# Kernel optimization log

Hardware: AMD Instinct MI355X
Metric: run time of the kernel (lower is better)

The kernel has to match this reference:

```python
import jax, jax.numpy as jnp
import numpy as np

N_NODES = 50000
N_EDGES = 800000
D_IN = 8
D_MODEL = 128
N_CLASSES = 2


def gcn_conv(x, W, b, src, dst, n_nodes):
    # PyG GCNConv: h = x @ W; add self-loops; D^{-1/2} A D^{-1/2} aggregation; + bias
    h = x @ W  # [N, D]
    deg = jax.ops.segment_sum(jnp.ones(src.shape[0], h.dtype), dst, num_segments=n_nodes) + 1.0  # +1 self-loop
    dinv = jax.lax.rsqrt(deg)  # deg >= 1 always
    norm = dinv[src] * dinv[dst]  # [E]
    agg = jax.ops.segment_sum(h[src] * norm[:, None], dst, num_segments=n_nodes)
    agg = agg + h * (dinv * dinv)[:, None]  # self-loop term, norm_ii = dinv_i^2
    return agg + b


def setup_inputs() -> dict:
    key = jax.random.key(0)
    ks = jax.random.split(key, 10)
    x = jax.random.normal(ks[0], (N_NODES, D_IN), jnp.float32)
    edge_index = jax.random.randint(ks[1], (2, N_EDGES), 0, N_NODES, jnp.int64 if jax.config.jax_enable_x64 else jnp.int32)
    def glorot(k, shape):
        lim = np.sqrt(6.0 / (shape[0] + shape[1]))
        return jax.random.uniform(k, shape, jnp.float32, -lim, lim)
    return {
        "x": x,
        "edge_index": edge_index,
        "W1": glorot(ks[2], (D_IN, D_MODEL)),
        "b1": jnp.zeros((D_MODEL,), jnp.float32),
        "W2": glorot(ks[3], (D_MODEL, D_MODEL)),
        "b2": jnp.zeros((D_MODEL,), jnp.float32),
        "Wlin1": glorot(ks[4], (2 * D_MODEL, D_MODEL)),
        "blin1": jnp.zeros((D_MODEL,), jnp.float32),
        "Wfin": glorot(ks[5], (D_MODEL, N_CLASSES)),
        "bfin": jnp.zeros((N_CLASSES,), jnp.float32),
    }


def reference(x, edge_index, W1, b1, W2, b2, Wlin1, blin1, Wfin, bfin):
    src, dst = edge_index[0], edge_index[1]
    n = x.shape[0]
    h = jax.nn.relu(gcn_conv(x, W1, b1, src, dst, n))
    h = jax.nn.relu(gcn_conv(h, W2, b2, src, dst, n))
    xpair = jnp.concatenate((h[src], h[dst]), axis=1)  # [E, 2*D]
    xpair = jax.nn.relu(xpair @ Wlin1 + blin1)
    logits = xpair @ Wfin + bfin  # [E, C]
    return jax.nn.log_softmax(logits, axis=1)
```

## Files before the change

kernel.cpp:

```cpp
#include <hip/hip_runtime.h>
#include <stdint.h>
#include <math.h>

#define D 128

typedef unsigned short u16;
typedef __attribute__((ext_vector_type(8))) short bf16x8;
typedef __attribute__((ext_vector_type(4))) float f32x4;
typedef __attribute__((ext_vector_type(2))) float f32x2;

union BU { uint4 u; bf16x8 s; };

__device__ __forceinline__ unsigned f2bf_pk(float a, float b) {
    union { float f; unsigned u; } x, y; x.f = a; y.f = b;
    unsigned ra = x.u + 0x7FFF + ((x.u >> 16) & 1);
    unsigned rb = y.u + 0x7FFF + ((y.u >> 16) & 1);
    return (ra >> 16) | (rb & 0xFFFF0000u);
}
__device__ __forceinline__ u16 f2bf(float f) {
    union { float f; unsigned u; } x; x.f = f;
    unsigned r = x.u + 0x7FFF + ((x.u >> 16) & 1);
    return (u16)(r >> 16);
}
__device__ __forceinline__ f32x2 bf2f2v(unsigned u) {
    union { unsigned w[2]; f32x2 v; } t;
    t.w[0] = u << 16; t.w[1] = u & 0xFFFF0000u;
    return t.v;
}
__device__ __forceinline__ f32x2 vmax0(f32x2 a) {
    return __builtin_elementwise_max(a, (f32x2)(0.f));
}
__device__ __forceinline__ int padded4(int deg) {
    return (deg + 3) & ~3;
}


__global__ __launch_bounds__(256) void k_degree8(const int* __restrict__ dst, int E,
                                                 int* __restrict__ hist8, int N) {
    int i = blockIdx.x * 256 + threadIdx.x;
    int copy = blockIdx.x & 7;
    int E4 = E >> 2;
    if (i < E4) {
        int4 d = ((const int4*)dst)[i];
        int* h = hist8 + copy * N;
        atomicAdd(&h[d.x], 1);
        atomicAdd(&h[d.y], 1);
        atomicAdd(&h[d.z], 1);
        atomicAdd(&h[d.w], 1);
    }
    if (i == 0) {
        for (int j = E4 * 4; j < E; ++j) atomicAdd(&hist8[dst[j]], 1);
    }
}

__global__ __launch_bounds__(256) void k_xcdoff_bsum(int* __restrict__ hist8, int* __restrict__ degi,
                                                     float* __restrict__ dinv, int* __restrict__ bsum, int N) {
    __shared__ int ws[4];
    int t = threadIdx.x;
    int i = blockIdx.x * 256 + t;
    int pd = 0;
    if (i < N) {
        int run = 0;
#pragma unroll
        for (int j = 0; j < 8; ++j) {
            int c = hist8[j * N + i];
            hist8[j * N + i] = run;
            run += c;
        }
        degi[i] = run;
        dinv[i] = rsqrtf((float)run + 1.0f);
        pd = padded4(run);
    }
    int v = pd;
#pragma unroll
    for (int off = 1; off < 64; off <<= 1) v += __shfl_xor(v, off, 64);
    if ((t & 63) == 0) ws[t >> 6] = v;
    __syncthreads();
    if (t == 0) bsum[blockIdx.x] = ws[0] + ws[1] + ws[2] + ws[3];
}

__global__ __launch_bounds__(1024) void k_boff_wprep(const int* __restrict__ bsum, int* __restrict__ boff,
                                                     int nb, int* __restrict__ prow, int N,
                                                     const float* __restrict__ W2, const float* __restrict__ Wlin,
                                                     unsigned* __restrict__ wswz) {
    int t = threadIdx.x;
    if (blockIdx.x == 0) {
        __shared__ int s[1024];
        s[t] = (t < nb) ? bsum[t] : 0;
        __syncthreads();
        for (int off = 1; off < 1024; off <<= 1) {
            int v = (t >= off) ? s[t - off] : 0;
            __syncthreads();
            s[t] += v;
            __syncthreads();
        }
        if (t < nb) boff[t] = (t == 0) ? 0 : s[t - 1];
        if (t == 0) prow[N] = s[1023];
    } else {
        int tid = (blockIdx.x - 1) * 1024 + t;
        int m = tid >> 13;
        int r = tid & 8191;
        int jp = r & 3;
        int lane = (r >> 2) & 63;
        int ct = (r >> 8) & 7;
        int kc = r >> 11;
        int k0 = kc * 32 + (lane >> 4) * 8 + 2 * jp;
        int n = ct * 16 + (lane & 15);
        const float* srcp = (m == 0) ? W2 : (Wlin + (m - 1) * 16384);
        wswz[tid] = f2bf_pk(srcp[k0 * 128 + n], srcp[(k0 + 1) * 128 + n]);
    }
}

__global__ __launch_bounds__(256) void k_scan_final(const int* __restrict__ degi, const int* __restrict__ boff,
                                                    int* __restrict__ prow, int N) {
    __shared__ int s[256];
    int t = threadIdx.x;
    int i = blockIdx.x * 256 + t;
    int pd = (i < N) ? padded4(degi[i]) : 0;
    s[t] = pd;
    __syncthreads();
    for (int off = 1; off < 256; off <<= 1) {
        int v = (t >= off) ? s[t - off] : 0;
        __syncthreads();
        s[t] += v;
        __syncthreads();
    }
    if (i < N) prow[i] = boff[blockIdx.x] + ((t == 0) ? 0 : s[t - 1]);
}


__global__ __launch_bounds__(256) void k_scatter_fill_xform(
        const int* __restrict__ src, const int* __restrict__ dst, int E,
        const int* __restrict__ prow, int* __restrict__ hist8, const int* __restrict__ degi,
        int2* __restrict__ coleid, int N, int eb4, int nb,
        const float* __restrict__ x, const float* __restrict__ W1,
        const float* __restrict__ dinv, unsigned* __restrict__ g) {
    __shared__ float Ws[8 * D];
    int t = threadIdx.x;
    int b = blockIdx.x;
    if (b < eb4) {
        int i = b * 256 + t;
        int copy = b & 7;
        int E4 = E >> 2;
        if (i < E4) {
            int4 d = ((const int4*)dst)[i];
            int4 s4 = ((const int4*)src)[i];
            int* h = hist8 + copy * N;
            int e = i * 4;
            int off;
            off = atomicAdd(&h[d.x], 1); coleid[prow[d.x] + off] = make_int2(s4.x, e + 0);
            off = atomicAdd(&h[d.y], 1); coleid[prow[d.y] + off] = make_int2(s4.y, e + 1);
            off = atomicAdd(&h[d.z], 1); coleid[prow[d.z] + off] = make_int2(s4.z, e + 2);
            off = atomicAdd(&h[d.w], 1); coleid[prow[d.w] + off] = make_int2(s4.w, e + 3);
        }
        if (i == 0) {
            for (int j = E4 * 4; j < E; ++j) {
                int d = dst[j];
                int off = atomicAdd(&hist8[d], 1);
                coleid[prow[d] + off] = make_int2(src[j], j);
            }
        }
    } else if (b < eb4 + nb) {
        int n = (b - eb4) * 256 + t;
        if (n < N) {
            int lo = prow[n];
            int deg = degi[n];
            int pd = padded4(deg);
            for (int j = deg; j < pd; ++j) coleid[lo + j] = make_int2(N, 0);
        }
        if (b == eb4 && t == 0) {
            int P = prow[N];
            for (int j = 0; j < 16; ++j) coleid[P + j] = make_int2(N, 0);
        }
    } else {
        int xb0 = b - eb4 - nb;
        for (int i = t; i < 8 * D; i += 256) Ws[i] = W1[i];
        __syncthreads();
        int node = xb0 * 4 + (t >> 6);
        int l = t & 63;
        if (node < N) {
            float s0 = 0.f, s1 = 0.f;
#pragma unroll
            for (int k = 0; k < 8; ++k) {
                float xv = x[node * 8 + k];
                s0 += xv * Ws[k * D + 2 * l];
                s1 += xv * Ws[k * D + 2 * l + 1];
            }
            float di = dinv[node];
            g[node * 64 + l] = f2bf_pk(s0 * di, s1 * di);
        }
        if (xb0 == 0 && t < 64) g[(size_t)N * 64 + t] = 0;
    }
}


#define HROW 136

template <bool DUAL>
__global__ __launch_bounds__(256) void k_aggemm(const uint4* __restrict__ g, const int* __restrict__ prow,
                                                const int2* __restrict__ coleid, const float* __restrict__ dinv,
                                                const float* __restrict__ biasH,
                                                const uint4* __restrict__ wB0, const uint4* __restrict__ wB1,
                                                const float* __restrict__ bias1,
                                                u16* __restrict__ out0, u16* __restrict__ out1, int N) {
    __shared__ u16 hs[16 * HROW];
    int t = threadIdx.x;
    int wv = t >> 6;
    int lane = t & 63;
    int sub = lane >> 4;
    int r = lane & 15;
    int base = blockIdx.x * 16;

    for (int nd = 0; nd < 4; ++nd) {
        int i = base + wv * 4 + nd;
        int lrow = wv * 4 + nd;
        if (i < N) {
            f32x2 acc2[4];
#pragma unroll
            for (int j = 0; j < 4; ++j) acc2[j] = (f32x2)(0.f);
            int lo = prow[i], hiP = prow[i + 1];
            int idx = lo + sub;
            int c0 = coleid[idx].x;
            int c1 = (idx + 4 < hiP) ? coleid[idx + 4].x : N;
            int c2 = (idx + 8 < hiP) ? coleid[idx + 8].x : N;
            uint4 v0 = g[c0 * 16 + r];
            uint4 v1 = g[c1 * 16 + r];
            for (int k = lo; k < hiP; k += 4) {
                int c3 = (idx + 12 < hiP) ? coleid[idx + 12].x : N;
                uint4 v2 = g[c2 * 16 + r];
                acc2[0] += bf2f2v(v0.x);
                acc2[1] += bf2f2v(v0.y);
                acc2[2] += bf2f2v(v0.z);
                acc2[3] += bf2f2v(v0.w);
                v0 = v1; v1 = v2; c2 = c3; idx += 4;
            }
#pragma unroll
            for (int j = 0; j < 4; ++j) {
                acc2[j].x += __shfl_xor(acc2[j].x, 16, 64);
                acc2[j].y += __shfl_xor(acc2[j].y, 16, 64);
                acc2[j].x += __shfl_xor(acc2[j].x, 32, 64);
                acc2[j].y += __shfl_xor(acc2[j].y, 32, 64);
            }
            if (sub == 0) {
                uint4 sv = g[i * 16 + r];
                acc2[0] += bf2f2v(sv.x);
                acc2[1] += bf2f2v(sv.y);
                acc2[2] += bf2f2v(sv.z);
                acc2[3] += bf2f2v(sv.w);
                float di = dinv[i];
                float4 b0 = ((const float4*)biasH)[r * 2];
                float4 b1v = ((const float4*)biasH)[r * 2 + 1];
                float r0 = fmaxf(acc2[0].x * di + b0.x, 0.f);
                float r1 = fmaxf(acc2[0].y * di + b0.y, 0.f);
                float r2 = fmaxf(acc2[1].x * di + b0.z, 0.f);
                float r3 = fmaxf(acc2[1].y * di + b0.w, 0.f);
                float r4 = fmaxf(acc2[2].x * di + b1v.x, 0.f);
                float r5 = fmaxf(acc2[2].y * di + b1v.y, 0.f);
                float r6 = fmaxf(acc2[3].x * di + b1v.z, 0.f);
                float r7 = fmaxf(acc2[3].y * di + b1v.w, 0.f);
                uint4 o;
                o.x = f2bf_pk(r0, r1);
                o.y = f2bf_pk(r2, r3);
                o.z = f2bf_pk(r4, r5);
                o.w = f2bf_pk(r6, r7);
                *(uint4*)(hs + lrow * HROW + r * 8) = o;
            }
        } else if (sub == 0) {
            *(uint4*)(hs + lrow * HROW + r * 8) = make_uint4(0, 0, 0, 0);
        }
    }
    __syncthreads();

    int quad = lane >> 4;
    int l15 = lane & 15;
    int ct0 = wv * 2;

    f32x4 accA[2], accB[2];
#pragma unroll
    for (int q = 0; q < 2; ++q) { accA[q] = (f32x4){0.f, 0.f, 0.f, 0.f}; accB[q] = (f32x4){0.f, 0.f, 0.f, 0.f}; }

    const uint4* hrow = (const uint4*)(hs + l15 * HROW);
#pragma unroll
    for (int kc = 0; kc < 4; ++kc) {
        BU a; a.u = hrow[kc * 4 + quad];
#pragma unroll
        for (int q = 0; q < 2; ++q) {
            BU b0; b0.u = wB0[(kc * 8 + ct0 + q) * 64 + lane];
            accA[q] = __builtin_amdgcn_mfma_f32_16x16x32_bf16(a.s, b0.s, accA[q], 0, 0, 0);
            if (DUAL) {
                BU b1; b1.u = wB1[(kc * 8 + ct0 + q) * 64 + lane];
                accB[q] = __builtin_amdgcn_mfma_f32_16x16x32_bf16(a.s, b1.s, accB[q], 0, 0, 0);
            }
        }
    }
#pragma unroll
    for (int reg = 0; reg < 4; ++reg) {
        int node = base + quad * 4 + reg;
        if (node >= N) continue;
        float sc = DUAL ? 1.0f : dinv[node];
#pragma unroll
        for (int q = 0; q < 2; ++q) {
            int colj = (ct0 + q) * 16 + l15;
            out0[(size_t)node * 128 + colj] = f2bf(accA[q][reg] * sc);
            if (DUAL) out1[(size_t)node * 128 + colj] = f2bf(accB[q][reg] + bias1[colj]);
        }
    }
    if (blockIdx.x == 0 && t < 64) ((unsigned*)out0)[(size_t)N * 64 + t] = 0;
}


__global__ __launch_bounds__(256) void k_edge(const uint4* __restrict__ a, const uint4* __restrict__ c,
                                              const int* __restrict__ prow, const int* __restrict__ degi,
                                              const int2* __restrict__ coleid,
                                              const float* __restrict__ Wfin, const float* __restrict__ bfin,
                                              float* __restrict__ out, int N) {
    int wave = (blockIdx.x * blockDim.x + threadIdx.x) >> 6;
    int lane = threadIdx.x & 63;
    if (wave >= N) return;
    int d = wave;
    int g = lane >> 4;
    int r = lane & 15;

    f32x2 wf0v[4], wf1v[4];
    const float4* wvp = (const float4*)Wfin;
#pragma unroll
    for (int q = 0; q < 4; ++q) {
        float4 m = wvp[r * 4 + q];
        wf0v[q] = (f32x2){m.x, m.z};
        wf1v[q] = (f32x2){m.y, m.w};
    }
    float bf0 = bfin[0], bf1 = bfin[1];

    f32x2 cf2[4];
    {
        uint4 cv = c[d * 16 + r];
        cf2[0] = bf2f2v(cv.x);
        cf2[1] = bf2f2v(cv.y);
        cf2[2] = bf2f2v(cv.z);
        cf2[3] = bf2f2v(cv.w);
    }

    int lo = prow[d], hiP = prow[d + 1];
    int deg = degi[d];

    int idx = lo + g;
    int2 q0 = coleid[idx];
    int2 q1 = coleid[idx + 4];
    int c1 = (idx + 4 < hiP) ? q1.x : N;
    int2 q2 = coleid[idx + 8];
    int c2 = (idx + 8 < hiP) ? q2.x : N;
    int e0 = q0.y, e1 = q1.y, e2 = q2.y;
    uint4 v0 = a[q0.x * 16 + r];
    uint4 v1 = a[c1 * 16 + r];

    int rel = g;
    for (int k = lo; k < hiP; k += 4) {
        int2 q3 = coleid[idx + 12];
        int c3 = (idx + 12 < hiP) ? q3.x : N;
        uint4 v2 = a[c2 * 16 + r];
        f32x2 p0v = (f32x2)(0.f), p1v = (f32x2)(0.f);
        f32x2 z;
        z = vmax0(bf2f2v(v0.x) + cf2[0]); p0v += z * wf0v[0]; p1v += z * wf1v[0];
        z = vmax0(bf2f2v(v0.y) + cf2[1]); p0v += z * wf0v[1]; p1v += z * wf1v[1];
        z = vmax0(bf2f2v(v0.z) + cf2[2]); p0v += z * wf0v[2]; p1v += z * wf1v[2];
        z = vmax0(bf2f2v(v0.w) + cf2[3]); p0v += z * wf0v[3]; p1v += z * wf1v[3];
        float p0 = p0v.x + p0v.y;
        float p1 = p1v.x + p1v.y;
        p0 += __shfl_xor(p0, 1, 64);
        p0 += __shfl_xor(p0, 2, 64);
        p0 += __shfl_xor(p0, 4, 64);
        p0 += __shfl_xor(p0, 8, 64);
        p1 += __shfl_xor(p1, 1, 64);
        p1 += __shfl_xor(p1, 2, 64);
        p1 += __shfl_xor(p1, 4, 64);
        p1 += __shfl_xor(p1, 8, 64);
        if (r == 0 && rel < deg) {
            float l0 = p0 + bf0, l1 = p1 + bf1;
            float m = fmaxf(l0, l1);
            float lse = m + __logf(__expf(l0 - m) + __expf(l1 - m));
            *((float2*)(out + 2 * (size_t)e0)) = make_float2(l0 - lse, l1 - lse);
        }
        v0 = v1; v1 = v2;
        e0 = e1; e1 = e2; e2 = q3.y;
        c2 = c3; idx += 4; rel += 4;
    }
}

extern "C" void kernel_launch(void* const* d_in, const int* in_sizes, int n_in,
                              void* d_out, int out_size, void* d_ws, size_t ws_size,
                              hipStream_t stream) {
    const float* x     = (const float*)d_in[0];
    const int*   ei    = (const int*)d_in[1];
    const float* W1    = (const float*)d_in[2];
    const float* b1    = (const float*)d_in[3];
    const float* W2    = (const float*)d_in[4];
    const float* b2    = (const float*)d_in[5];
    const float* Wlin1 = (const float*)d_in[6];
    const float* blin1 = (const float*)d_in[7];
    const float* Wfin  = (const float*)d_in[8];
    const float* bfin  = (const float*)d_in[9];
    float* out = (float*)d_out;

    int N = in_sizes[0] / 8;
    int E = in_sizes[1] / 2;
    const int* src = ei;
    const int* dst = ei + E;
    int nb = (N + 255) / 256;
    int eb4 = (E / 4 + 255) / 256;
    int xb = (N + 3) / 4;

    char* w = (char*)d_ws;
    int* hist8 = (int*)w;     w += (size_t)8 * N * 4;
    int* degi = (int*)w;      w += (size_t)N * 4;
    int* prow = (int*)w;      w += (size_t)(N + 1) * 4;
    float* dinv = (float*)w;  w += (size_t)N * 4;
    int* bsum = (int*)w;      w += (size_t)nb * 4;
    int* boff = (int*)w;      w += (size_t)nb * 4;
    w = (char*)(((uintptr_t)w + 255) & ~(uintptr_t)255);
    int2* coleid = (int2*)w;  w += ((size_t)E + 8 * (size_t)N + 64) * 8;
    unsigned* wswz = (unsigned*)w; w += (size_t)3 * 8192 * 4;
    unsigned* bufG = (unsigned*)w; w += (size_t)(N + 1) * 64 * 4;
    unsigned* bufA = (unsigned*)w; w += (size_t)(N + 1) * 64 * 4;
    unsigned* bufC = (unsigned*)w; w += (size_t)N * 64 * 4;
    unsigned* bufG2 = (unsigned*)w; w += (size_t)(N + 1) * 64 * 4;

    hipMemsetAsync(hist8, 0, (size_t)8 * N * 4, stream);

    k_degree8<<<eb4, 256, 0, stream>>>(dst, E, hist8, N);
    k_xcdoff_bsum<<<nb, 256, 0, stream>>>(hist8, degi, dinv, bsum, N);
    k_boff_wprep<<<25, 1024, 0, stream>>>(bsum, boff, nb, prow, N, W2, Wlin1, wswz);
    k_scan_final<<<nb, 256, 0, stream>>>(degi, boff, prow, N);
    k_scatter_fill_xform<<<eb4 + nb + xb, 256, 0, stream>>>(src, dst, E, prow, hist8, degi,
                                                            coleid, N, eb4, nb, x, W1, dinv, bufG);

    int ablocks = (N + 15) / 16;
    k_aggemm<false><<<ablocks, 256, 0, stream>>>((const uint4*)bufG, prow, coleid, dinv, b1,
                                                 (const uint4*)wswz, nullptr, nullptr,
                                                 (u16*)bufG2, nullptr, N);
    k_aggemm<true><<<ablocks, 256, 0, stream>>>((const uint4*)bufG2, prow, coleid, dinv, b2,
                                                (const uint4*)(wswz + 8192), (const uint4*)(wswz + 16384),
                                                blin1, (u16*)bufA, (u16*)bufC, N);

    k_edge<<<(N + 3) / 4, 256, 0, stream>>>((const uint4*)bufA, (const uint4*)bufC,
                                            prow, degi, coleid, Wfin, bfin, out, N);
}
```

Baseline: 294.3 us.

## Replace 8 private degree histograms with destination-range-partitioned single histogram

Instead of eight replicated histogram copies (one per block group) that must be prefix-combined, each edge chunk is now read by eight blocks, each owning one eighth of the destination-node range and doing atomics only into that slice of a single histogram. This removes the 8xN histogram memset, the per-node combine pass and the degi array, and keeps each part's atomics within a narrow address range, presumably to improve L2 locality per XCD. In exchange the dst array is read eight times, and src is read once for each part that has a hit, both in the degree pass and the scatter pass.

```diff
diff --git a/kernel.cpp b/kernel.cpp
--- a/kernel.cpp
+++ b/kernel.cpp
@@ -35,39 +35,32 @@
 }
 
 
-__global__ __launch_bounds__(256) void k_degree8(const int* __restrict__ dst, int E,
-                                                 int* __restrict__ hist8, int N) {
-    int i = blockIdx.x * 256 + threadIdx.x;
-    int copy = blockIdx.x & 7;
-    int E4 = E >> 2;
-    if (i < E4) {
+__global__ __launch_bounds__(256) void k_degree_part(const int* __restrict__ dst, int E,
+                                                     int* __restrict__ hist, int N8, int G4) {
+    int b = blockIdx.x;
+    int part = b & 7;
+    int i = (b >> 3) * 256 + threadIdx.x;
+    int lo = part * N8;
+    if (i < G4) {
         int4 d = ((const int4*)dst)[i];
-        int* h = hist8 + copy * N;
-        atomicAdd(&h[d.x], 1);
-        atomicAdd(&h[d.y], 1);
-        atomicAdd(&h[d.z], 1);
-        atomicAdd(&h[d.w], 1);
-    }
-    if (i == 0) {
-        for (int j = E4 * 4; j < E; ++j) atomicAdd(&hist8[dst[j]], 1);
-    }
-}
-
-__global__ __launch_bounds__(256) void k_xcdoff_bsum(int* __restrict__ hist8, int* __restrict__ degi,
-                                                     float* __restrict__ dinv, int* __restrict__ bsum, int N) {
+        if ((unsigned)(d.x - lo) < (unsigned)N8) atomicAdd(&hist[d.x], 1);
+        if ((unsigned)(d.y - lo) < (unsigned)N8) atomicAdd(&hist[d.y], 1);
+        if ((unsigned)(d.z - lo) < (unsigned)N8) atomicAdd(&hist[d.z], 1);
+        if ((unsigned)(d.w - lo) < (unsigned)N8) atomicAdd(&hist[d.w], 1);
+    }
+    if (b == 0 && threadIdx.x == 0) {
+        for (int j = G4 * 4; j < E; ++j) atomicAdd(&hist[dst[j]], 1);
+    }
+}
+
+__global__ __launch_bounds__(256) void k_dinv_bsum(const int* __restrict__ hist,
+                                                   float* __restrict__ dinv, int* __restrict__ bsum, int N) {
     __shared__ int ws[4];
     int t = threadIdx.x;
     int i = blockIdx.x * 256 + t;
     int pd = 0;
     if (i < N) {
-        int run = 0;
-#pragma unroll
-        for (int j = 0; j < 8; ++j) {
-            int c = hist8[j * N + i];
-            hist8[j * N + i] = run;
-            run += c;
-        }
-        degi[i] = run;
+        int run = hist[i];
         dinv[i] = rsqrtf((float)run + 1.0f);
         pd = padded4(run);
     }
@@ -111,12 +104,12 @@
     }
 }
 
-__global__ __launch_bounds__(256) void k_scan_final(const int* __restrict__ degi, const int* __restrict__ boff,
+__global__ __launch_bounds__(256) void k_scan_final(const int* __restrict__ hist, const int* __restrict__ boff,
                                                     int* __restrict__ prow, int N) {
     __shared__ int s[256];
     int t = threadIdx.x;
     int i = blockIdx.x * 256 + t;
-    int pd = (i < N) ? padded4(degi[i]) : 0;
+    int pd = (i < N) ? padded4(hist[i]) : 0;
     s[t] = pd;
     __syncthreads();
     for (int off = 1; off < 256; off <<= 1) {
@@ -131,49 +124,54 @@
 
 __global__ __launch_bounds__(256) void k_scatter_fill_xform(
         const int* __restrict__ src, const int* __restrict__ dst, int E,
-        const int* __restrict__ prow, int* __restrict__ hist8, const int* __restrict__ degi,
-        int2* __restrict__ coleid, int N, int eb4, int nb,
+        const int* __restrict__ prow, int* __restrict__ cursor, const int* __restrict__ hist,
+        int2* __restrict__ coleid, int N, int N8, int G4, int sgrid, int nb,
         const float* __restrict__ x, const float* __restrict__ W1,
         const float* __restrict__ dinv, unsigned* __restrict__ g) {
     __shared__ float Ws[8 * D];
     int t = threadIdx.x;
     int b = blockIdx.x;
-    if (b < eb4) {
-        int i = b * 256 + t;
-        int copy = b & 7;
-        int E4 = E >> 2;
-        if (i < E4) {
+    if (b < sgrid) {
+        int part = b & 7;
+        int i = (b >> 3) * 256 + t;
+        int lo = part * N8;
+        if (i < G4) {
             int4 d = ((const int4*)dst)[i];
-            int4 s4 = ((const int4*)src)[i];
-            int* h = hist8 + copy * N;
-            int e = i * 4;
-            int off;
-            off = atomicAdd(&h[d.x], 1); coleid[prow[d.x] + off] = make_int2(s4.x, e + 0);
-            off = atomicAdd(&h[d.y], 1); coleid[prow[d.y] + off] = make_int2(s4.y, e + 1);
-            off = atomicAdd(&h[d.z], 1); coleid[prow[d.z] + off] = make_int2(s4.z, e + 2);
-            off = atomicAdd(&h[d.w], 1); coleid[prow[d.w] + off] = make_int2(s4.w, e + 3);
-        }
-        if (i == 0) {
-            for (int j = E4 * 4; j < E; ++j) {
+            bool h0 = (unsigned)(d.x - lo) < (unsigned)N8;
+            bool h1 = (unsigned)(d.y - lo) < (unsigned)N8;
+            bool h2 = (unsigned)(d.z - lo) < (unsigned)N8;
+            bool h3 = (unsigned)(d.w - lo) < (unsigned)N8;
+            if (h0 | h1 | h2 | h3) {
+                int4 s4 = ((const int4*)src)[i];
+                int e = i * 4;
+                int off;
+                if (h0) { off = atomicAdd(&cursor[d.x], 1); coleid[prow[d.x] + off] = make_int2(s4.x, e + 0); }
+                if (h1) { off = atomicAdd(&cursor[d.y], 1); coleid[prow[d.y] + off] = make_int2(s4.y, e + 1); }
+                if (h2) { off = atomicAdd(&cursor[d.z], 1); coleid[prow[d.z] + off] = make_int2(s4.z, e + 2); }
+                if (h3) { off = atomicAdd(&cursor[d.w], 1); coleid[prow[d.w] + off] = make_int2(s4.w, e + 3); }
+            }
+        }
+        if (b == 0 && t == 0) {
+            for (int j = G4 * 4; j < E; ++j) {
                 int d = dst[j];
-                int off = atomicAdd(&hist8[d], 1);
+                int off = atomicAdd(&cursor[d], 1);
                 coleid[prow[d] + off] = make_int2(src[j], j);
             }
         }
-    } else if (b < eb4 + nb) {
-        int n = (b - eb4) * 256 + t;
+    } else if (b < sgrid + nb) {
+        int n = (b - sgrid) * 256 + t;
         if (n < N) {
             int lo = prow[n];
-            int deg = degi[n];
+            int deg = hist[n];
             int pd = padded4(deg);
             for (int j = deg; j < pd; ++j) coleid[lo + j] = make_int2(N, 0);
         }
-        if (b == eb4 && t == 0) {
+        if (b == sgrid && t == 0) {
             int P = prow[N];
             for (int j = 0; j < 16; ++j) coleid[P + j] = make_int2(N, 0);
         }
     } else {
-        int xb0 = b - eb4 - nb;
+        int xb0 = b - sgrid - nb;
         for (int i = t; i < 8 * D; i += 256) Ws[i] = W1[i];
         __syncthreads();
         int node = xb0 * 4 + (t >> 6);
@@ -406,12 +404,15 @@
     const int* src = ei;
     const int* dst = ei + E;
     int nb = (N + 255) / 256;
-    int eb4 = (E / 4 + 255) / 256;
     int xb = (N + 3) / 4;
+    int N8 = (N + 7) / 8;
+    int G4 = E >> 2;
+    int ngc = (G4 + 255) / 256;
+    int sgrid = ngc * 8;
 
     char* w = (char*)d_ws;
-    int* hist8 = (int*)w;     w += (size_t)8 * N * 4;
-    int* degi = (int*)w;      w += (size_t)N * 4;
+    int* hist = (int*)w;      w += (size_t)N * 4;
+    int* cursor = (int*)w;    w += (size_t)N * 4;
     int* prow = (int*)w;      w += (size_t)(N + 1) * 4;
     float* dinv = (float*)w;  w += (size_t)N * 4;
     int* bsum = (int*)w;      w += (size_t)nb * 4;
@@ -424,14 +425,15 @@
     unsigned* bufC = (unsigned*)w; w += (size_t)N * 64 * 4;
     unsigned* bufG2 = (unsigned*)w; w += (size_t)(N + 1) * 64 * 4;
 
-    hipMemsetAsync(hist8, 0, (size_t)8 * N * 4, stream);
-
-    k_degree8<<<eb4, 256, 0, stream>>>(dst, E, hist8, N);
-    k_xcdoff_bsum<<<nb, 256, 0, stream>>>(hist8, degi, dinv, bsum, N);
+    hipMemsetAsync(hist, 0, (size_t)2 * N * 4, stream);
+
+    k_degree_part<<<sgrid, 256, 0, stream>>>(dst, E, hist, N8, G4);
+    k_dinv_bsum<<<nb, 256, 0, stream>>>(hist, dinv, bsum, N);
     k_boff_wprep<<<25, 1024, 0, stream>>>(bsum, boff, nb, prow, N, W2, Wlin1, wswz);
-    k_scan_final<<<nb, 256, 0, stream>>>(degi, boff, prow, N);
-    k_scatter_fill_xform<<<eb4 + nb + xb, 256, 0, stream>>>(src, dst, E, prow, hist8, degi,
-                                                            coleid, N, eb4, nb, x, W1, dinv, bufG);
+    k_scan_final<<<nb, 256, 0, stream>>>(hist, boff, prow, N);
+    k_scatter_fill_xform<<<sgrid + nb + xb, 256, 0, stream>>>(src, dst, E, prow, cursor, hist,
+                                                              coleid, N, N8, G4, sgrid, nb,
+                                                              x, W1, dinv, bufG);
 
     int ablocks = (N + 15) / 16;
     k_aggemm<false><<<ablocks, 256, 0, stream>>>((const uint4*)bufG, prow, coleid, dinv, b1,
@@ -442,5 +444,5 @@
                                                 blin1, (u16*)bufA, (u16*)bufC, N);
 
     k_edge<<<(N + 3) / 4, 256, 0, stream>>>((const uint4*)bufA, (const uint4*)bufC,
-                                            prow, degi, coleid, Wfin, bfin, out, N);
-}
+                                            prow, hist, coleid, Wfin, bfin, out, N);
+}
```

Result: no change. 296.7 us (+0.8%).
